# Optimization experiments

Measured on AMD Instinct MI355X. Metric: run time of the kernel, lower is better.

## Reference

```python
import jax, jax.numpy as jnp
import numpy as np

SR = 16000.0
WIN = 400
SHIFT = 160
NMEL = 80
PREEMPH = 0.97
EPS = float(np.finfo(np.float64).eps)


def _mel_banks(num_bins, win, sr):
    # kaldi-compatible triangular mel banks, low_freq=20, high_freq=nyquist
    def hz2mel(f):
        return 1127.0 * np.log(1.0 + f / 700.0)
    mlow, mhigh = hz2mel(20.0), hz2mel(sr / 2.0)
    d = (mhigh - mlow) / (num_bins + 1)
    left = mlow + np.arange(num_bins) * d
    center = left + d
    right = left + 2 * d
    fft_freqs = (sr / win) * np.arange(win // 2)
    mel = hz2mel(fft_freqs)[None, :]
    up = (mel - left[:, None]) / d
    down = (right[:, None] - mel) / d
    banks = np.maximum(0.0, np.minimum(up, down))
    banks = np.concatenate([banks, np.zeros((num_bins, 1))], axis=1)  # pad last rfft bin
    return jnp.asarray(banks, jnp.float32)

_BANKS = _mel_banks(NMEL, WIN, SR)
_WINDOW = jnp.asarray(0.5 - 0.5 * np.cos(2 * np.pi * np.arange(WIN) / (WIN - 1)), jnp.float32)


def setup_inputs() -> dict:
    key = jax.random.key(0)
    k1, k2 = jax.random.split(key)
    B, L = 64, 240000
    x = jax.random.normal(k1, (B, L), dtype=jnp.float32)
    T = jax.random.randint(k2, (B,), 1, L, dtype=jnp.int32)
    normalizer = jnp.full((NMEL,), 0.1, dtype=jnp.float32)  # Parameter init 1/10
    return {"x": x, "T": T, "normalizer": normalizer}


def _fbank(x, normalizer):
    B, L = x.shape
    n_frames = 1 + (L - WIN) // SHIFT  # snip_edges=True
    idx = np.arange(n_frames)[:, None] * SHIFT + np.arange(WIN)[None, :]
    frames = x[:, idx]
    # preemphasis: frame[i] -= 0.97 * frame[i-1]; first sample uses itself
    prev = jnp.concatenate([frames[..., :1], frames[..., :-1]], axis=-1)
    frames = (frames - PREEMPH * prev) * _WINDOW
    spec = jnp.abs(jnp.fft.rfft(frames, axis=-1)) ** 2
    mel = jnp.einsum('bfk,mk->bfm', spec, _BANKS)
    mel = jnp.log(jnp.maximum(mel, EPS))
    return mel * normalizer[None, None, :]


def reference(x, T, normalizer):
    fb = _fbank(x, normalizer)                            # (B, F, M)
    B, F, M = fb.shape
    # faithful to source: downsample_factor = max(T) / fbanks[0].shape[1] (= num_mel_bins)
    ds = jnp.max(T).astype(jnp.float32) / M
    T_ = (T.astype(jnp.float32) / ds).astype(jnp.int32)   # int() truncation, T >= 0
    mask = (jnp.arange(F)[None, :] < T_[:, None])[..., None]  # (B, F, 1)
    cnt = jnp.maximum(T_, 1).astype(fb.dtype)[:, None, None]
    mean = jnp.sum(jnp.where(mask, fb, 0.0), axis=1, keepdims=True) / cnt
    return jnp.where(mask, fb - mean, fb)
```

## Files before the change

### kernel.cpp

```cpp
#include <hip/hip_runtime.h>
#include <hip/hip_bf16.h>

#define BATCH   64
#define LSIG    240000
#define WIN     400
#define SHIFT   160
#define NFR     1498
#define NMEL    80
#define NBIN    200
#define NF      8
#define MAXW    14
#define SPECW   (NBIN + MAXW)

__device__ float g_win[WIN];
__device__ float g_tw1[11][20][2];
__device__ float g_tw2[NBIN][20][2];
__device__ int   g_melStart[NMEL];
__device__ float g_melW[NMEL][MAXW];

__global__ void init_tables_kernel() {
    const int tid = threadIdx.x;
    const double PI = 3.14159265358979323846;
    __shared__ double melf[NBIN];

    for (int t = tid; t < WIN; t += 256)
        g_win[t] = (float)(0.5 - 0.5 * cos(2.0 * PI * (double)t / 399.0));

    for (int i = tid; i < 11 * 20; i += 256) {
        int r = i / 20, t1 = i % 20;
        double th = -2.0 * PI * (double)(r * t1) / 20.0;
        g_tw1[r][t1][0] = (float)cos(th);
        g_tw1[r][t1][1] = (float)sin(th);
    }
    for (int i = tid; i < NBIN * 20; i += 256) {
        int k = i / 20, t2 = i % 20;
        double th = -2.0 * PI * (double)(k * t2) / 400.0;
        g_tw2[k][t2][0] = (float)cos(th);
        g_tw2[k][t2][1] = (float)sin(th);
    }
    for (int k = tid; k < NBIN; k += 256)
        melf[k] = 1127.0 * log(1.0 + (40.0 * (double)k) / 700.0);
    __syncthreads();

    if (tid < NMEL) {
        int m = tid;
        double mlow  = 1127.0 * log(1.0 + 20.0   / 700.0);
        double mhigh = 1127.0 * log(1.0 + 8000.0 / 700.0);
        double d     = (mhigh - mlow) / (double)(NMEL + 1);
        double inv_d = 1.0 / d;
        double left  = mlow + (double)m * d;
        double right = left + 2.0 * d;
        for (int j = 0; j < MAXW; j++) g_melW[m][j] = 0.0f;
        int start = 0; bool found = false;
        for (int k = 0; k < NBIN; k++) {
            double up = (melf[k] - left) * inv_d, down = (right - melf[k]) * inv_d;
            double w = fmax(0.0, fmin(up, down));
            if (w > 0.0) {
                if (!found) { start = k; found = true; }
                int j = k - start;
                if (j < MAXW) g_melW[m][j] = (float)w;
            }
        }
        g_melStart[m] = start;
    }
}

__global__ __launch_bounds__(256, 6)
void fbank_kernel(const float* __restrict__ x, const float* __restrict__ norm,
                  float* __restrict__ out) {
    const int ft = blockIdx.x;
    const int b  = blockIdx.y;
    const int f0 = ft * NF;
    const int nf = min(NF, NFR - f0);

    __shared__ __align__(16) float smem[3520 + NF * SPECW];
    float* Sb   = smem;
    float* xseg = smem + 3520;
    float* spec = smem + 3520;

    const float* xb = x + (size_t)b * LSIG + (size_t)f0 * SHIFT;
    const int seglen = (nf - 1) * SHIFT + WIN;
    for (int i = threadIdx.x; i < seglen; i += 256) xseg[i] = xb[i];
    __syncthreads();

    {
        const int p = threadIdx.x;
        if (p < nf * 20) {
            const int f = p / 20, t2 = p - f * 20;
            const float* xf = xseg + f * SHIFT;
            float yr[20];
#pragma unroll
            for (int t1 = 0; t1 < 20; t1++) {
                int t = t2 + 20 * t1;
                float xc = xf[t];
                float xp = xf[t > 0 ? t - 1 : 0];
                yr[t1] = (xc - 0.97f * xp) * g_win[t];
            }
#pragma unroll
            for (int r = 0; r <= 10; r++) {
                float ar = 0.0f, ai = 0.0f;
#pragma unroll
                for (int t1 = 0; t1 < 20; t1++) {
                    float c = g_tw1[r][t1][0], s = g_tw1[r][t1][1];
                    ar = fmaf(yr[t1], c, ar);
                    ai = fmaf(yr[t1], s, ai);
                }
                *(float2*)(Sb + ((f * 11 + r) * 20 + t2) * 2) = make_float2(ar, ai);
            }
        }
    }
    __syncthreads();

    {
        const int k = threadIdx.x;
        if (k < NBIN) {
            int r = k % 20;
            bool cj = (r > 10);
            int rp = cj ? 20 - r : r;
            float sgn = cj ? -1.0f : 1.0f;
            float twc[20], s2[20];
#pragma unroll
            for (int t2 = 0; t2 < 20; t2++) {
                twc[t2] = g_tw2[k][t2][0];
                s2[t2]  = g_tw2[k][t2][1] * sgn;
            }
            for (int f = 0; f < nf; f++) {
                const float4* Sf = (const float4*)(Sb + (f * 11 + rp) * 40);
                float xr0 = 0.f, xi0 = 0.f, xr1 = 0.f, xi1 = 0.f;
#pragma unroll
                for (int q = 0; q < 10; q++) {
                    float4 v = Sf[q];
                    float c0 = twc[2 * q],     ss0 = s2[2 * q];
                    float c1 = twc[2 * q + 1], ss1 = s2[2 * q + 1];
                    xr0 = fmaf(c0, v.x, xr0);  xr0 = fmaf(-ss0, v.y, xr0);
                    xi0 = fmaf(ss0, v.x, xi0); xi0 = fmaf(c0,  v.y, xi0);
                    xr1 = fmaf(c1, v.z, xr1);  xr1 = fmaf(-ss1, v.w, xr1);
                    xi1 = fmaf(ss1, v.z, xi1); xi1 = fmaf(c1,  v.w, xi1);
                }
                float xr = xr0 + xr1, xi = xi0 + xi1;
                spec[f * SPECW + k] = fmaf(xr, xr, xi * xi);
            }
        } else if (k < NBIN + MAXW) {
            for (int f = 0; f < nf; f++) spec[f * SPECW + k] = 0.0f;
        }
    }
    __syncthreads();

    const int outs = nf * NMEL;
    for (int o = threadIdx.x; o < outs; o += 256) {
        int f = o / NMEL, m = o - f * NMEL;
        int ks = g_melStart[m];
        const float* sp = spec + f * SPECW + ks;
        float acc = 0.0f;
#pragma unroll
        for (int j = 0; j < MAXW; j++)
            acc = fmaf(g_melW[m][j], sp[j], acc);
        float mel = fmaxf(acc, 2.2204460492503131e-16f);
        float v = logf(mel) * norm[m];
        out[((size_t)b * NFR + (f0 + f)) * NMEL + m] = v;
    }
}

__global__ __launch_bounds__(256)
void meansub_kernel(float* __restrict__ out, const int* __restrict__ T) {
    const int b = blockIdx.x;
    __shared__ float part[3][NMEL];
    __shared__ float meanSh[NMEL];

    int maxT = T[0];
    for (int i = 1; i < BATCH; i++) maxT = max(maxT, T[i]);
    float ds = (float)maxT / (float)NMEL;
    int tb = (int)((float)T[b] / ds);

    const int q = threadIdx.x / NMEL;
    const int m = threadIdx.x - q * NMEL;
    float* pb = out + (size_t)b * NFR * NMEL;

    if (q < 3) {
        float s = 0.0f;
        for (int f = q; f < tb; f += 3) s += pb[(size_t)f * NMEL + m];
        part[q][m] = s;
    }
    __syncthreads();
    if (threadIdx.x < NMEL) {
        float mean = (part[0][m] + part[1][m] + part[2][m]) / (float)max(tb, 1);
        meanSh[m] = mean;
    }
    __syncthreads();
    if (q < 3) {
        float mean = meanSh[m];
        for (int f = q; f < tb; f += 3) pb[(size_t)f * NMEL + m] -= mean;
    }
}

extern "C" void kernel_launch(void* const* d_in, const int* in_sizes, int n_in,
                              void* d_out, int out_size, void* d_ws, size_t ws_size,
                              hipStream_t stream) {
    const float* x    = (const float*)d_in[0];
    const int*   T    = (const int*)d_in[1];
    const float* norm = (const float*)d_in[2];
    float* out = (float*)d_out;

    init_tables_kernel<<<1, 256, 0, stream>>>();

    dim3 grid((NFR + NF - 1) / NF, BATCH);
    fbank_kernel<<<grid, 256, 0, stream>>>(x, norm, out);

    meansub_kernel<<<BATCH, 256, 0, stream>>>(out, T);
}
```

Baseline: 227.6 us.

## Transpose twiddle and stage-1 layouts, interchange stage-2 loops over frames

Twiddle tables are now built from a shared 400-entry root table instead of per-entry double-precision trig calls. The second-stage twiddles are transposed so that consecutive k threads read coalesced float2 values. The stage-1 shared buffer is reordered to [f][t2][r]. Stage 2 now loops over t2 on the outside and keeps eight frame accumulators in registers, so each twiddle is loaded once and reused across frames. This trades the float4 shared reads for float2 reads and adds register pressure. It also always computes all NF frames, even when a tile holds fewer.

```diff
diff --git a/kernel.cpp b/kernel.cpp
--- a/kernel.cpp
+++ b/kernel.cpp
@@ -14,7 +14,7 @@
 
 __device__ float g_win[WIN];
 __device__ float g_tw1[11][20][2];
-__device__ float g_tw2[NBIN][20][2];
+__device__ float g_tw2T[20][NBIN][2];
 __device__ int   g_melStart[NMEL];
 __device__ float g_melW[NMEL][MAXW];
 
@@ -22,26 +22,30 @@
     const int tid = threadIdx.x;
     const double PI = 3.14159265358979323846;
     __shared__ double melf[NBIN];
-
-    for (int t = tid; t < WIN; t += 256)
-        g_win[t] = (float)(0.5 - 0.5 * cos(2.0 * PI * (double)t / 399.0));
+    __shared__ float root[WIN][2];
+
+    for (int j = tid; j < WIN; j += 256) {
+        double th = -2.0 * PI * (double)j / 400.0;
+        root[j][0] = (float)cos(th);
+        root[j][1] = (float)sin(th);
+        g_win[j] = (float)(0.5 - 0.5 * cos(2.0 * PI * (double)j / 399.0));
+    }
+    for (int k = tid; k < NBIN; k += 256)
+        melf[k] = 1127.0 * log(1.0 + (40.0 * (double)k) / 700.0);
+    __syncthreads();
 
     for (int i = tid; i < 11 * 20; i += 256) {
         int r = i / 20, t1 = i % 20;
-        double th = -2.0 * PI * (double)(r * t1) / 20.0;
-        g_tw1[r][t1][0] = (float)cos(th);
-        g_tw1[r][t1][1] = (float)sin(th);
+        int j = (20 * r * t1) % 400;
+        g_tw1[r][t1][0] = root[j][0];
+        g_tw1[r][t1][1] = root[j][1];
     }
     for (int i = tid; i < NBIN * 20; i += 256) {
-        int k = i / 20, t2 = i % 20;
-        double th = -2.0 * PI * (double)(k * t2) / 400.0;
-        g_tw2[k][t2][0] = (float)cos(th);
-        g_tw2[k][t2][1] = (float)sin(th);
-    }
-    for (int k = tid; k < NBIN; k += 256)
-        melf[k] = 1127.0 * log(1.0 + (40.0 * (double)k) / 700.0);
-    __syncthreads();
-
+        int t2 = i / NBIN, k = i - t2 * NBIN;
+        int j = (k * t2) % 400;
+        g_tw2T[t2][k][0] = root[j][0];
+        g_tw2T[t2][k][1] = root[j][1];
+    }
     if (tid < NMEL) {
         int m = tid;
         double mlow  = 1127.0 * log(1.0 + 20.0   / 700.0);
@@ -105,7 +109,7 @@
                     ar = fmaf(yr[t1], c, ar);
                     ai = fmaf(yr[t1], s, ai);
                 }
-                *(float2*)(Sb + ((f * 11 + r) * 20 + t2) * 2) = make_float2(ar, ai);
+                *(float2*)(Sb + ((f * 20 + t2) * 11 + r) * 2) = make_float2(ar, ai);
             }
         }
     }
@@ -115,31 +119,24 @@
         const int k = threadIdx.x;
         if (k < NBIN) {
             int r = k % 20;
-            bool cj = (r > 10);
-            int rp = cj ? 20 - r : r;
-            float sgn = cj ? -1.0f : 1.0f;
-            float twc[20], s2[20];
-#pragma unroll
+            int rp  = (r > 10) ? 20 - r : r;
+            float sg = (r > 10) ? -1.0f : 1.0f;
+            float xr[NF], xi[NF];
+#pragma unroll
+            for (int f = 0; f < NF; f++) { xr[f] = 0.0f; xi[f] = 0.0f; }
+            const float2* twp = (const float2*)&g_tw2T[0][k][0];
             for (int t2 = 0; t2 < 20; t2++) {
-                twc[t2] = g_tw2[k][t2][0];
-                s2[t2]  = g_tw2[k][t2][1] * sgn;
-            }
-            for (int f = 0; f < nf; f++) {
-                const float4* Sf = (const float4*)(Sb + (f * 11 + rp) * 40);
-                float xr0 = 0.f, xi0 = 0.f, xr1 = 0.f, xi1 = 0.f;
-#pragma unroll
-                for (int q = 0; q < 10; q++) {
-                    float4 v = Sf[q];
-                    float c0 = twc[2 * q],     ss0 = s2[2 * q];
-                    float c1 = twc[2 * q + 1], ss1 = s2[2 * q + 1];
-                    xr0 = fmaf(c0, v.x, xr0);  xr0 = fmaf(-ss0, v.y, xr0);
-                    xi0 = fmaf(ss0, v.x, xi0); xi0 = fmaf(c0,  v.y, xi0);
-                    xr1 = fmaf(c1, v.z, xr1);  xr1 = fmaf(-ss1, v.w, xr1);
-                    xi1 = fmaf(ss1, v.z, xi1); xi1 = fmaf(c1,  v.w, xi1);
+                float2 tw = twp[t2 * NBIN];
+                float c = tw.x, s = tw.y * sg;
+#pragma unroll
+                for (int f = 0; f < NF; f++) {
+                    float2 v = *(const float2*)(Sb + ((f * 20 + t2) * 11 + rp) * 2);
+                    xr[f] = fmaf(c, v.x, fmaf(-s, v.y, xr[f]));
+                    xi[f] = fmaf(s, v.x, fmaf(c,  v.y, xi[f]));
                 }
-                float xr = xr0 + xr1, xi = xi0 + xi1;
-                spec[f * SPECW + k] = fmaf(xr, xr, xi * xi);
-            }
+            }
+            for (int f = 0; f < nf; f++)
+                spec[f * SPECW + k] = fmaf(xr[f], xr[f], xi[f] * xi[f]);
         } else if (k < NBIN + MAXW) {
             for (int f = 0; f < nf; f++) spec[f * SPECW + k] = 0.0f;
         }
@@ -182,10 +179,8 @@
         part[q][m] = s;
     }
     __syncthreads();
-    if (threadIdx.x < NMEL) {
-        float mean = (part[0][m] + part[1][m] + part[2][m]) / (float)max(tb, 1);
-        meanSh[m] = mean;
-    }
+    if (threadIdx.x < NMEL)
+        meanSh[m] = (part[0][m] + part[1][m] + part[2][m]) / (float)max(tb, 1);
     __syncthreads();
     if (q < 3) {
         float mean = meanSh[m];
```

Result: slower. 232.5 us (+2.2%).
